# Kernel optimization log

Hardware: AMD Instinct MI355X
Metric: run time of the kernel (lower is better)

Reference implementation:

```python
import jax, jax.numpy as jnp
import numpy as np

DIM_NODE = 128
DIM_EDGE = 128
DIM_TIME = 100
NUM_HEAD = 8
DIM_OUT = 128
LN_EPS = 1e-5


def setup_inputs() -> dict:
    key = jax.random.key(0)
    ks = jax.random.split(key, 12)
    D, E = 25000, 250000
    src_feat = jax.random.normal(ks[0], (D + E, DIM_NODE), jnp.float32)
    edge_f = jax.random.normal(ks[1], (E, DIM_EDGE), jnp.float32)
    edge_dt = jax.random.uniform(ks[2], (E,), jnp.float32)
    src_idx = jnp.arange(D + E, dtype=jnp.int64)
    edge_dst = jnp.sort(jax.random.randint(ks[3], (E,), 0, D)).astype(jnp.int64)
    # TimeEncode params (fixed init from the module)
    time_w = jnp.asarray(1.0 / 10 ** np.linspace(0, 9, DIM_TIME, dtype=np.float32))  # (DIM_TIME,)
    time_b = jnp.zeros((DIM_TIME,), jnp.float32)
    dq = DIM_NODE + DIM_TIME           # 228
    dkv = DIM_NODE + DIM_EDGE + DIM_TIME  # 356
    s = 0.05
    wq_w = jax.random.normal(ks[4], (DIM_OUT, dq), jnp.float32) * s
    wq_b = jnp.zeros((DIM_OUT,), jnp.float32)
    wk_w = jax.random.normal(ks[5], (DIM_OUT, dkv), jnp.float32) * s
    wk_b = jnp.zeros((DIM_OUT,), jnp.float32)
    wv_w = jax.random.normal(ks[6], (DIM_OUT, dkv), jnp.float32) * s
    wv_b = jnp.zeros((DIM_OUT,), jnp.float32)
    wout_w = jax.random.normal(ks[7], (DIM_OUT, DIM_NODE + DIM_OUT), jnp.float32) * s
    wout_b = jnp.zeros((DIM_OUT,), jnp.float32)
    ln_g = jnp.ones((DIM_OUT,), jnp.float32)
    ln_b = jnp.zeros((DIM_OUT,), jnp.float32)
    return dict(src_feat=src_feat, edge_f=edge_f, edge_dt=edge_dt,
                time_w=time_w, time_b=time_b,
                wq_w=wq_w, wq_b=wq_b, wk_w=wk_w, wk_b=wk_b,
                wv_w=wv_w, wv_b=wv_b, wout_w=wout_w, wout_b=wout_b,
                ln_g=ln_g, ln_b=ln_b, src_idx=src_idx, edge_dst=edge_dst)


def reference(src_feat, edge_f, edge_dt, time_w, time_b,
              wq_w, wq_b, wk_w, wk_b, wv_w, wv_b,
              wout_w, wout_b, ln_g, ln_b, src_idx, edge_dst):
    E = edge_f.shape[0]
    src_data = src_feat[src_idx]              # (D+E, dn)
    D = src_data.shape[0] - E
    q_data = src_data[:D]                     # (D, dn)
    kv_data = src_data[D:]                    # (E, dn)

    # TimeEncode: cos(w * t + b)
    time_feat = jnp.cos(edge_dt[:, None] * time_w[None, :] + time_b)       # (E, dt)
    zero_time_feat = jnp.broadcast_to(jnp.cos(time_b), (D, DIM_TIME))      # (D, dt)

    Qd = jnp.concatenate([q_data, zero_time_feat], axis=1) @ wq_w.T + wq_b  # (D, dout)
    Q = Qd[edge_dst]                                                        # (E, dout)
    kv_in = jnp.concatenate([kv_data, edge_f, time_feat], axis=1)           # (E, dkv)
    K = kv_in @ wk_w.T + wk_b
    V = kv_in @ wv_w.T + wv_b

    dh = DIM_OUT // NUM_HEAD
    Q = Q.reshape(E, NUM_HEAD, dh)
    K = K.reshape(E, NUM_HEAD, dh)
    V = V.reshape(E, NUM_HEAD, dh)

    scores = jax.nn.leaky_relu(jnp.sum(Q * K, axis=2), 0.2)   # (E, H)
    # edge softmax: segment softmax over dst nodes
    m = jax.ops.segment_max(scores, edge_dst, num_segments=D)  # (D, H)
    m = jnp.where(jnp.isfinite(m), m, 0.0)
    ex = jnp.exp(scores - m[edge_dst])
    den = jax.ops.segment_sum(ex, edge_dst, num_segments=D)    # (D, H)
    att = ex / den[edge_dst]                                    # (E, H)

    Vw = (V * att[:, :, None]).reshape(E, DIM_OUT)
    h = jax.ops.segment_sum(Vw, edge_dst, num_segments=D)       # (D, dout)

    rst = jnp.concatenate([h, q_data], axis=1) @ wout_w.T + wout_b
    rst = jax.nn.relu(rst)
    mu = jnp.mean(rst, axis=-1, keepdims=True)
    var = jnp.var(rst, axis=-1, keepdims=True)
    return (rst - mu) / jnp.sqrt(var + LN_EPS) * ln_g + ln_b
```

## Files before the change

kernel.cpp:

```cpp
#include <hip/hip_runtime.h>
#include <stdint.h>

#define DIM_TIME 100
#define DQ 228
#define DKV 356
#define KPAD 384
#define NB 256
#define BM 64
#define BK 32
#define NCHUNK 12
#define A_STRIDE 392
#define C_STRIDE 264

typedef short v8s __attribute__((ext_vector_type(8)));
typedef float v4f __attribute__((ext_vector_type(4)));

__device__ __forceinline__ unsigned short bf16_bits(float f) {
    union { float f; uint32_t u; } c; c.f = f;
    uint32_t u = c.u;
    uint32_t r = (u + 0x7FFFu + ((u >> 16) & 1u)) >> 16;
    return (unsigned short)r;
}
__device__ __forceinline__ float bf16_lo(uint32_t u) {
    union { uint32_t u; float f; } c; c.u = u << 16; return c.f;
}
__device__ __forceinline__ float bf16_hi(uint32_t u) {
    union { uint32_t u; float f; } c; c.u = u & 0xFFFF0000u; return c.f;
}

__global__ void prep_wt2(const float* __restrict__ wk_w, const float* __restrict__ wv_w,
                         unsigned short* __restrict__ Wt2) {
    int n = blockIdx.x;
    int k = threadIdx.x;
    float v = 0.f;
    if (k < DKV) v = (n < 128) ? wk_w[n * DKV + k] : wv_w[(n - 128) * DKV + k];
    Wt2[n * KPAD + k] = bf16_bits(v);
}

__global__ void prep_wqt(const float* __restrict__ wq_w, float* __restrict__ Wqt) {
    int k = blockIdx.x, o = threadIdx.x;
    Wqt[k * 128 + o] = wq_w[o * DQ + k];
}

__global__ void prep_wot(const float* __restrict__ wout_w, float* __restrict__ Wot) {
    int k = blockIdx.x, o = threadIdx.x;
    Wot[k * 128 + o] = wout_w[o * 256 + k];
}

__global__ void prep_cq(const float* __restrict__ wq_w, const float* __restrict__ wq_b,
                        const float* __restrict__ time_b, float* __restrict__ cq) {
    int o = threadIdx.x;
    float s = wq_b[o];
    for (int t = 0; t < DIM_TIME; ++t)
        s += cosf(time_b[t]) * wq_w[o * DQ + 128 + t];
    cq[o] = s;
}

__global__ __launch_bounds__(256) void qd_kernel(
        const float* __restrict__ src_feat, const int* __restrict__ src_idx,
        const float* __restrict__ Wqt, const float* __restrict__ cq,
        float* __restrict__ Qd, int D) {
    __shared__ float q_s[32][128];
    int lane = threadIdx.x & 63, wave = threadIdx.x >> 6;
    int r0 = wave * 8;
    int d0 = blockIdx.x * 32 + r0;
    #pragma unroll
    for (int i = 0; i < 8; ++i) {
        int d = d0 + i;
        float v0 = 0.f, v1 = 0.f;
        if (d < D) {
            const float* p = src_feat + (size_t)src_idx[d] * 128;
            v0 = p[lane]; v1 = p[lane + 64];
        }
        q_s[r0 + i][lane] = v0; q_s[r0 + i][lane + 64] = v1;
    }
    float c0 = cq[lane], c1 = cq[lane + 64];
    float acc0[8], acc1[8];
    #pragma unroll
    for (int i = 0; i < 8; ++i) { acc0[i] = c0; acc1[i] = c1; }
    #pragma unroll 8
    for (int k = 0; k < 128; ++k) {
        float w0 = Wqt[k * 128 + lane];
        float w1 = Wqt[k * 128 + 64 + lane];
        #pragma unroll
        for (int i = 0; i < 8; ++i) {
            float a = q_s[r0 + i][k];
            acc0[i] += a * w0; acc1[i] += a * w1;
        }
    }
    #pragma unroll
    for (int i = 0; i < 8; ++i) {
        int d = d0 + i;
        if (d < D) {
            Qd[(size_t)d * 128 + lane]      = acc0[i];
            Qd[(size_t)d * 128 + 64 + lane] = acc1[i];
        }
    }
}

__global__ __launch_bounds__(256) void kv_mfma(
        const float* __restrict__ src_feat, const int* __restrict__ src_idx,
        const float* __restrict__ edge_f, const float* __restrict__ edge_dt,
        const float* __restrict__ time_w, const float* __restrict__ time_b,
        const unsigned short* __restrict__ Wt2,
        const float* __restrict__ wk_b, const float* __restrict__ wv_b,
        unsigned short* __restrict__ KVb, int D, int E) {
    __shared__ unsigned short A_s[BM * A_STRIDE];
    int tid = threadIdx.x;
    int e0 = blockIdx.x * BM;
    int lane = tid & 63, wave = tid >> 6;
    int l15 = lane & 15, quad = lane >> 4;
    int wn = wave * 64;

    {
        int row = tid >> 2;
        int cb  = (tid & 3) * 8;
        int e = e0 + row;
        bool ok = (e < E);
        size_t nbase = ok ? (size_t)src_idx[D + e] * 128 : 0;
        #pragma unroll
        for (int i = 0; i < 8; ++i) {
            int c4 = cb + i;
            float4 v = ok ? *(const float4*)(src_feat + nbase + c4 * 4)
                          : make_float4(0.f, 0.f, 0.f, 0.f);
            ushort4 w;
            w.x = bf16_bits(v.x); w.y = bf16_bits(v.y);
            w.z = bf16_bits(v.z); w.w = bf16_bits(v.w);
            *(ushort4*)&A_s[row * A_STRIDE + c4 * 4] = w;
        }
        #pragma unroll
        for (int i = 0; i < 8; ++i) {
            int c4 = cb + i;
            float4 v = ok ? *(const float4*)(edge_f + (size_t)e * 128 + c4 * 4)
                          : make_float4(0.f, 0.f, 0.f, 0.f);
            ushort4 w;
            w.x = bf16_bits(v.x); w.y = bf16_bits(v.y);
            w.z = bf16_bits(v.z); w.w = bf16_bits(v.w);
            *(ushort4*)&A_s[row * A_STRIDE + 128 + c4 * 4] = w;
        }
    }
    {
        int c = tid & 127;
        int rbase = tid >> 7;
        bool vc = (c < DIM_TIME);
        float tw = vc ? time_w[c] : 0.f;
        float tb = vc ? time_b[c] : 0.f;
        #pragma unroll
        for (int i = 0; i < 32; ++i) {
            int row = i * 2 + rbase;
            int e = e0 + row;
            float v = 0.f;
            if (vc && e < E) v = __cosf(edge_dt[e] * tw + tb);
            A_s[row * A_STRIDE + 256 + c] = bf16_bits(v);
        }
    }
    __syncthreads();

    v4f acc[4][4];
    #pragma unroll
    for (int mf = 0; mf < 4; ++mf)
        #pragma unroll
        for (int nf = 0; nf < 4; ++nf)
            acc[mf][nf] = (v4f)(0.f);

    const unsigned short* wp = Wt2 + (size_t)(wn + l15) * KPAD + quad * 8;
    const unsigned short* ap = A_s + l15 * A_STRIDE + quad * 8;

    v8s bcur[4], acur[4];
    #pragma unroll
    for (int nf = 0; nf < 4; ++nf) bcur[nf] = *(const v8s*)(wp + nf * 16 * KPAD);
    #pragma unroll
    for (int mf = 0; mf < 4; ++mf) acur[mf] = *(const v8s*)(ap + mf * 16 * A_STRIDE);

    #pragma unroll 2
    for (int ch = 0; ch < NCHUNK; ++ch) {
        int k2 = (ch + 1 < NCHUNK) ? (ch + 1) * BK : 0;
        v8s bn[4], an[4];
        #pragma unroll
        for (int nf = 0; nf < 4; ++nf) bn[nf] = *(const v8s*)(wp + nf * 16 * KPAD + k2);
        #pragma unroll
        for (int mf = 0; mf < 4; ++mf) an[mf] = *(const v8s*)(ap + mf * 16 * A_STRIDE + k2);
        #pragma unroll
        for (int mf = 0; mf < 4; ++mf)
            #pragma unroll
            for (int nf = 0; nf < 4; ++nf)
                acc[mf][nf] = __builtin_amdgcn_mfma_f32_16x16x32_bf16(
                                  acur[mf], bcur[nf], acc[mf][nf], 0, 0, 0);
        #pragma unroll
        for (int nf = 0; nf < 4; ++nf) bcur[nf] = bn[nf];
        #pragma unroll
        for (int mf = 0; mf < 4; ++mf) acur[mf] = an[mf];
    }

    __syncthreads();
    #pragma unroll
    for (int nf = 0; nf < 4; ++nf) {
        int n = wn + nf * 16 + l15;
        float bias = (n < 128) ? wk_b[n] : wv_b[n - 128];
        #pragma unroll
        for (int mf = 0; mf < 4; ++mf)
            #pragma unroll
            for (int r = 0; r < 4; ++r)
                A_s[(mf * 16 + quad * 4 + r) * C_STRIDE + n] =
                    bf16_bits(acc[mf][nf][r] + bias);
    }
    __syncthreads();
    #pragma unroll
    for (int j = 0; j < 8; ++j) {
        int c = j * 256 + tid;
        int row = c >> 5;
        int col = (c & 31) * 8;
        if (e0 + row < E) {
            v8s v = *(const v8s*)&A_s[row * C_STRIDE + col];
            *(v8s*)&KVb[(size_t)(e0 + row) * NB + col] = v;
        }
    }
}

__global__ void seg_offsets(const int* __restrict__ edge_dst, int* __restrict__ start,
                            int D, int E) {
    int d = blockIdx.x * blockDim.x + threadIdx.x;
    if (d > D) return;
    int lo = 0, hi = E;
    while (lo < hi) {
        int mid = (lo + hi) >> 1;
        if (edge_dst[mid] < d) lo = mid + 1; else hi = mid;
    }
    start[d] = lo;
}

__global__ __launch_bounds__(256) void attn_kernel(
        const float* __restrict__ Qd, const unsigned short* __restrict__ KVb,
        const int* __restrict__ start, float* __restrict__ h, int D) {
    int lane = threadIdx.x & 63, wave = threadIdx.x >> 6;
    int dbase = blockIdx.x * 16 + wave * 4;
    for (int i = 0; i < 4; ++i) {
        int d = dbase + i;
        if (d >= D) break;
        float2 q = *(const float2*)(Qd + (size_t)d * 128 + lane * 2);
        int s0 = start[d], s1 = start[d + 1];
        float m = -INFINITY, l = 0.f, a0 = 0.f, a1 = 0.f;
        for (int e = s0; e < s1; ++e) {
            const unsigned short* kv = KVb + (size_t)e * 256 + lane * 2;
            uint32_t ku = *(const uint32_t*)kv;
            uint32_t vu = *(const uint32_t*)(kv + 128);
            float qk = q.x * bf16_lo(ku) + q.y * bf16_hi(ku);
            qk += __shfl_xor(qk, 4, 8);
            qk += __shfl_xor(qk, 2, 8);
            qk += __shfl_xor(qk, 1, 8);
            float s = qk > 0.f ? qk : 0.2f * qk;
            float nm = fmaxf(m, s);
            float sc = __expf(m - nm);
            float p  = __expf(s - nm);
            l  = l  * sc + p;
            a0 = a0 * sc + p * bf16_lo(vu);
            a1 = a1 * sc + p * bf16_hi(vu);
            m = nm;
        }
        float inv = (l > 0.f) ? 1.f / l : 0.f;
        *(float2*)(h + (size_t)d * 128 + lane * 2) = make_float2(a0 * inv, a1 * inv);
    }
}

__global__ __launch_bounds__(256) void out_kernel(
        const float* __restrict__ h, const float* __restrict__ src_feat,
        const int* __restrict__ src_idx, const float* __restrict__ Wot,
        const float* __restrict__ wout_b, const float* __restrict__ ln_g,
        const float* __restrict__ ln_b, float* __restrict__ out, int D) {
    __shared__ float in_s[32][256];
    int lane = threadIdx.x & 63, wave = threadIdx.x >> 6;
    int r0 = wave * 8;
    int d0 = blockIdx.x * 32 + r0;
    #pragma unroll
    for (int i = 0; i < 8; ++i) {
        int d = d0 + i;
        float a0 = 0.f, a1 = 0.f, b0 = 0.f, b1 = 0.f;
        if (d < D) {
            const float* ph = h + (size_t)d * 128;
            a0 = ph[lane]; a1 = ph[lane + 64];
            const float* pf = src_feat + (size_t)src_idx[d] * 128;
            b0 = pf[lane]; b1 = pf[lane + 64];
        }
        in_s[r0 + i][lane] = a0; in_s[r0 + i][lane + 64] = a1;
        in_s[r0 + i][128 + lane] = b0; in_s[r0 + i][192 + lane] = b1;
    }
    float bb0 = wout_b[lane], bb1 = wout_b[lane + 64];
    float acc0[8], acc1[8];
    #pragma unroll
    for (int i = 0; i < 8; ++i) { acc0[i] = bb0; acc1[i] = bb1; }
    #pragma unroll 8
    for (int k = 0; k < 256; ++k) {
        float w0 = Wot[k * 128 + lane];
        float w1 = Wot[k * 128 + 64 + lane];
        #pragma unroll
        for (int i = 0; i < 8; ++i) {
            float a = in_s[r0 + i][k];
            acc0[i] += a * w0; acc1[i] += a * w1;
        }
    }
    float g0 = ln_g[lane], g1 = ln_g[lane + 64];
    float lb0 = ln_b[lane], lb1 = ln_b[lane + 64];
    #pragma unroll
    for (int i = 0; i < 8; ++i) {
        float v0 = fmaxf(acc0[i], 0.f), v1 = fmaxf(acc1[i], 0.f);
        float s1 = v0 + v1, s2 = v0 * v0 + v1 * v1;
        #pragma unroll
        for (int off = 32; off; off >>= 1) {
            s1 += __shfl_xor(s1, off);
            s2 += __shfl_xor(s2, off);
        }
        float mu  = s1 * (1.f / 128.f);
        float var = s2 * (1.f / 128.f) - mu * mu;
        float rs  = rsqrtf(var + 1e-5f);
        int d = d0 + i;
        if (d < D) {
            out[(size_t)d * 128 + lane]      = (v0 - mu) * rs * g0 + lb0;
            out[(size_t)d * 128 + 64 + lane] = (v1 - mu) * rs * g1 + lb1;
        }
    }
}

extern "C" void kernel_launch(void* const* d_in, const int* in_sizes, int n_in,
                              void* d_out, int out_size, void* d_ws, size_t ws_size,
                              hipStream_t stream) {
    const float* src_feat = (const float*)d_in[0];
    const float* edge_f   = (const float*)d_in[1];
    const float* edge_dt  = (const float*)d_in[2];
    const float* time_w   = (const float*)d_in[3];
    const float* time_b   = (const float*)d_in[4];
    const float* wq_w     = (const float*)d_in[5];
    const float* wq_b     = (const float*)d_in[6];
    const float* wk_w     = (const float*)d_in[7];
    const float* wk_b     = (const float*)d_in[8];
    const float* wv_w     = (const float*)d_in[9];
    const float* wv_b     = (const float*)d_in[10];
    const float* wout_w   = (const float*)d_in[11];
    const float* wout_b   = (const float*)d_in[12];
    const float* ln_g     = (const float*)d_in[13];
    const float* ln_b     = (const float*)d_in[14];
    const int*   src_idx  = (const int*)d_in[15];
    const int*   edge_dst = (const int*)d_in[16];

    int DE = in_sizes[0] / 128;
    int E  = in_sizes[1] / 128;
    int D  = DE - E;

    char* ws = (char*)d_ws;
    size_t off = 0;
    auto alloc = [&](size_t bytes) {
        void* p = ws + off;
        off = (off + bytes + 511) & ~(size_t)511;
        return p;
    };
    unsigned short* Wt2   = (unsigned short*)alloc((size_t)NB * KPAD * 2);
    float*          Wqt   = (float*)alloc(128 * 128 * 4);
    float*          Wot   = (float*)alloc(256 * 128 * 4);
    float*          cq    = (float*)alloc(128 * 4);
    float*          Qd    = (float*)alloc((size_t)D * 128 * 4);
    unsigned short* KVb   = (unsigned short*)alloc((size_t)E * 256 * 2);
    float*          hb    = (float*)alloc((size_t)D * 128 * 4);
    int*            start = (int*)alloc((size_t)(D + 1) * 4);

    hipLaunchKernelGGL(prep_wt2, dim3(NB), dim3(KPAD), 0, stream, wk_w, wv_w, Wt2);
    hipLaunchKernelGGL(prep_wqt, dim3(128), dim3(128), 0, stream, wq_w, Wqt);
    hipLaunchKernelGGL(prep_wot, dim3(256), dim3(128), 0, stream, wout_w, Wot);
    hipLaunchKernelGGL(prep_cq, dim3(1), dim3(128), 0, stream, wq_w, wq_b, time_b, cq);
    hipLaunchKernelGGL(qd_kernel, dim3((D + 31) / 32), dim3(256), 0, stream,
                       src_feat, src_idx, Wqt, cq, Qd, D);
    hipLaunchKernelGGL(kv_mfma, dim3((E + BM - 1) / BM), dim3(256), 0, stream,
                       src_feat, src_idx, edge_f, edge_dt, time_w, time_b,
                       Wt2, wk_b, wv_b, KVb, D, E);
    hipLaunchKernelGGL(seg_offsets, dim3((D + 1 + 255) / 256), dim3(256), 0, stream,
                       edge_dst, start, D, E);
    hipLaunchKernelGGL(attn_kernel, dim3((D + 15) / 16), dim3(256), 0, stream,
                       Qd, KVb, start, hb, D);
    hipLaunchKernelGGL(out_kernel, dim3((D + 31) / 32), dim3(256), 0, stream,
                       hb, src_feat, src_idx, Wot, wout_b, ln_g, ln_b, (float*)d_out, D);
}
```

Baseline: 640.0 us.

## Halve KV GEMM tile rows, batch attention KV loads, vectorize small GEMM loads

The KV projection kernel now uses 32-row tiles instead of 64, which doubles the block count and gives more blocks per CU for latency hiding, at the cost of reusing each weight fragment less. The attention kernel issues up to four edges' K/V loads before the serial online-softmax updates, so memory latency overlaps across edges. The Q and output projection kernels switch to float2 loads and stores for weights, biases and outputs, with each lane now owning adjacent column pairs. The launch config for the KV kernel presumably already derives its grid from BM.

```diff
diff --git a/kernel.cpp b/kernel.cpp
--- a/kernel.cpp
+++ b/kernel.cpp
@@ -6,7 +6,7 @@
 #define DKV 356
 #define KPAD 384
 #define NB 256
-#define BM 64
+#define BM 32
 #define BK 32
 #define NCHUNK 12
 #define A_STRIDE 392
@@ -74,27 +74,24 @@
         }
         q_s[r0 + i][lane] = v0; q_s[r0 + i][lane + 64] = v1;
     }
-    float c0 = cq[lane], c1 = cq[lane + 64];
+    float2 c2 = *(const float2*)(cq + 2 * lane);
     float acc0[8], acc1[8];
     #pragma unroll
-    for (int i = 0; i < 8; ++i) { acc0[i] = c0; acc1[i] = c1; }
+    for (int i = 0; i < 8; ++i) { acc0[i] = c2.x; acc1[i] = c2.y; }
     #pragma unroll 8
     for (int k = 0; k < 128; ++k) {
-        float w0 = Wqt[k * 128 + lane];
-        float w1 = Wqt[k * 128 + 64 + lane];
+        float2 w = *(const float2*)(Wqt + k * 128 + 2 * lane);
         #pragma unroll
         for (int i = 0; i < 8; ++i) {
             float a = q_s[r0 + i][k];
-            acc0[i] += a * w0; acc1[i] += a * w1;
+            acc0[i] += a * w.x; acc1[i] += a * w.y;
         }
     }
     #pragma unroll
     for (int i = 0; i < 8; ++i) {
         int d = d0 + i;
-        if (d < D) {
-            Qd[(size_t)d * 128 + lane]      = acc0[i];
-            Qd[(size_t)d * 128 + 64 + lane] = acc1[i];
-        }
+        if (d < D)
+            *(float2*)(Qd + (size_t)d * 128 + 2 * lane) = make_float2(acc0[i], acc1[i]);
     }
 }
 
@@ -113,13 +110,13 @@
     int wn = wave * 64;
 
     {
-        int row = tid >> 2;
-        int cb  = (tid & 3) * 8;
+        int row = tid >> 3;
+        int cb  = (tid & 7) * 4;
         int e = e0 + row;
         bool ok = (e < E);
         size_t nbase = ok ? (size_t)src_idx[D + e] * 128 : 0;
         #pragma unroll
-        for (int i = 0; i < 8; ++i) {
+        for (int i = 0; i < 4; ++i) {
             int c4 = cb + i;
             float4 v = ok ? *(const float4*)(src_feat + nbase + c4 * 4)
                           : make_float4(0.f, 0.f, 0.f, 0.f);
@@ -129,7 +126,7 @@
             *(ushort4*)&A_s[row * A_STRIDE + c4 * 4] = w;
         }
         #pragma unroll
-        for (int i = 0; i < 8; ++i) {
+        for (int i = 0; i < 4; ++i) {
             int c4 = cb + i;
             float4 v = ok ? *(const float4*)(edge_f + (size_t)e * 128 + c4 * 4)
                           : make_float4(0.f, 0.f, 0.f, 0.f);
@@ -146,7 +143,7 @@
         float tw = vc ? time_w[c] : 0.f;
         float tb = vc ? time_b[c] : 0.f;
         #pragma unroll
-        for (int i = 0; i < 32; ++i) {
+        for (int i = 0; i < 16; ++i) {
             int row = i * 2 + rbase;
             int e = e0 + row;
             float v = 0.f;
@@ -156,9 +153,9 @@
     }
     __syncthreads();
 
-    v4f acc[4][4];
-    #pragma unroll
-    for (int mf = 0; mf < 4; ++mf)
+    v4f acc[2][4];
+    #pragma unroll
+    for (int mf = 0; mf < 2; ++mf)
         #pragma unroll
         for (int nf = 0; nf < 4; ++nf)
             acc[mf][nf] = (v4f)(0.f);
@@ -166,22 +163,22 @@
     const unsigned short* wp = Wt2 + (size_t)(wn + l15) * KPAD + quad * 8;
     const unsigned short* ap = A_s + l15 * A_STRIDE + quad * 8;
 
-    v8s bcur[4], acur[4];
+    v8s bcur[4], acur[2];
     #pragma unroll
     for (int nf = 0; nf < 4; ++nf) bcur[nf] = *(const v8s*)(wp + nf * 16 * KPAD);
     #pragma unroll
-    for (int mf = 0; mf < 4; ++mf) acur[mf] = *(const v8s*)(ap + mf * 16 * A_STRIDE);
+    for (int mf = 0; mf < 2; ++mf) acur[mf] = *(const v8s*)(ap + mf * 16 * A_STRIDE);
 
     #pragma unroll 2
     for (int ch = 0; ch < NCHUNK; ++ch) {
         int k2 = (ch + 1 < NCHUNK) ? (ch + 1) * BK : 0;
-        v8s bn[4], an[4];
+        v8s bn[4], an[2];
         #pragma unroll
         for (int nf = 0; nf < 4; ++nf) bn[nf] = *(const v8s*)(wp + nf * 16 * KPAD + k2);
         #pragma unroll
-        for (int mf = 0; mf < 4; ++mf) an[mf] = *(const v8s*)(ap + mf * 16 * A_STRIDE + k2);
-        #pragma unroll
-        for (int mf = 0; mf < 4; ++mf)
+        for (int mf = 0; mf < 2; ++mf) an[mf] = *(const v8s*)(ap + mf * 16 * A_STRIDE + k2);
+        #pragma unroll
+        for (int mf = 0; mf < 2; ++mf)
             #pragma unroll
             for (int nf = 0; nf < 4; ++nf)
                 acc[mf][nf] = __builtin_amdgcn_mfma_f32_16x16x32_bf16(
@@ -189,7 +186,7 @@
         #pragma unroll
         for (int nf = 0; nf < 4; ++nf) bcur[nf] = bn[nf];
         #pragma unroll
-        for (int mf = 0; mf < 4; ++mf) acur[mf] = an[mf];
+        for (int mf = 0; mf < 2; ++mf) acur[mf] = an[mf];
     }
 
     __syncthreads();
@@ -198,7 +195,7 @@
         int n = wn + nf * 16 + l15;
         float bias = (n < 128) ? wk_b[n] : wv_b[n - 128];
         #pragma unroll
-        for (int mf = 0; mf < 4; ++mf)
+        for (int mf = 0; mf < 2; ++mf)
             #pragma unroll
             for (int r = 0; r < 4; ++r)
                 A_s[(mf * 16 + quad * 4 + r) * C_STRIDE + n] =
@@ -206,7 +203,7 @@
     }
     __syncthreads();
     #pragma unroll
-    for (int j = 0; j < 8; ++j) {
+    for (int j = 0; j < 4; ++j) {
         int c = j * 256 + tid;
         int row = c >> 5;
         int col = (c & 31) * 8;
@@ -240,22 +237,31 @@
         float2 q = *(const float2*)(Qd + (size_t)d * 128 + lane * 2);
         int s0 = start[d], s1 = start[d + 1];
         float m = -INFINITY, l = 0.f, a0 = 0.f, a1 = 0.f;
-        for (int e = s0; e < s1; ++e) {
-            const unsigned short* kv = KVb + (size_t)e * 256 + lane * 2;
-            uint32_t ku = *(const uint32_t*)kv;
-            uint32_t vu = *(const uint32_t*)(kv + 128);
-            float qk = q.x * bf16_lo(ku) + q.y * bf16_hi(ku);
-            qk += __shfl_xor(qk, 4, 8);
-            qk += __shfl_xor(qk, 2, 8);
-            qk += __shfl_xor(qk, 1, 8);
-            float s = qk > 0.f ? qk : 0.2f * qk;
-            float nm = fmaxf(m, s);
-            float sc = __expf(m - nm);
-            float p  = __expf(s - nm);
-            l  = l  * sc + p;
-            a0 = a0 * sc + p * bf16_lo(vu);
-            a1 = a1 * sc + p * bf16_hi(vu);
-            m = nm;
+        for (int e = s0; e < s1; e += 4) {
+            int n = s1 - e; if (n > 4) n = 4;
+            uint32_t ku[4], vu[4];
+            #pragma unroll
+            for (int j = 0; j < 4; ++j) {
+                if (j < n) {
+                    const unsigned short* kv = KVb + (size_t)(e + j) * 256 + lane * 2;
+                    ku[j] = *(const uint32_t*)kv;
+                    vu[j] = *(const uint32_t*)(kv + 128);
+                }
+            }
+            for (int j = 0; j < n; ++j) {
+                float qk = q.x * bf16_lo(ku[j]) + q.y * bf16_hi(ku[j]);
+                qk += __shfl_xor(qk, 4, 8);
+                qk += __shfl_xor(qk, 2, 8);
+                qk += __shfl_xor(qk, 1, 8);
+                float s = qk > 0.f ? qk : 0.2f * qk;
+                float nm = fmaxf(m, s);
+                float sc = __expf(m - nm);
+                float p  = __expf(s - nm);
+                l  = l  * sc + p;
+                a0 = a0 * sc + p * bf16_lo(vu[j]);
+                a1 = a1 * sc + p * bf16_hi(vu[j]);
+                m = nm;
+            }
         }
         float inv = (l > 0.f) ? 1.f / l : 0.f;
         *(float2*)(h + (size_t)d * 128 + lane * 2) = make_float2(a0 * inv, a1 * inv);
@@ -284,22 +290,21 @@
         in_s[r0 + i][lane] = a0; in_s[r0 + i][lane + 64] = a1;
         in_s[r0 + i][128 + lane] = b0; in_s[r0 + i][192 + lane] = b1;
     }
-    float bb0 = wout_b[lane], bb1 = wout_b[lane + 64];
+    float2 bb = *(const float2*)(wout_b + 2 * lane);
     float acc0[8], acc1[8];
     #pragma unroll
-    for (int i = 0; i < 8; ++i) { acc0[i] = bb0; acc1[i] = bb1; }
+    for (int i = 0; i < 8; ++i) { acc0[i] = bb.x; acc1[i] = bb.y; }
     #pragma unroll 8
     for (int k = 0; k < 256; ++k) {
-        float w0 = Wot[k * 128 + lane];
-        float w1 = Wot[k * 128 + 64 + lane];
+        float2 w = *(const float2*)(Wot + k * 128 + 2 * lane);
         #pragma unroll
         for (int i = 0; i < 8; ++i) {
             float a = in_s[r0 + i][k];
-            acc0[i] += a * w0; acc1[i] += a * w1;
-        }
-    }
-    float g0 = ln_g[lane], g1 = ln_g[lane + 64];
-    float lb0 = ln_b[lane], lb1 = ln_b[lane + 64];
+            acc0[i] += a * w.x; acc1[i] += a * w.y;
+        }
+    }
+    float2 g = *(const float2*)(ln_g + 2 * lane);
+    float2 lb = *(const float2*)(ln_b + 2 * lane);
     #pragma unroll
     for (int i = 0; i < 8; ++i) {
         float v0 = fmaxf(acc0[i], 0.f), v1 = fmaxf(acc1[i], 0.f);
@@ -313,10 +318,9 @@
         float var = s2 * (1.f / 128.f) - mu * mu;
         float rs  = rsqrtf(var + 1e-5f);
         int d = d0 + i;
-        if (d < D) {
-            out[(size_t)d * 128 + lane]      = (v0 - mu) * rs * g0 + lb0;
-            out[(size_t)d * 128 + 64 + lane] = (v1 - mu) * rs * g1 + lb1;
-        }
+        if (d < D)
+            *(float2*)(out + (size_t)d * 128 + 2 * lane) =
+                make_float2((v0 - mu) * rs * g.x + lb.x, (v1 - mu) * rs * g.y + lb.y);
     }
 }
 
```

Measured after the change: 672.8 us. 5.1% more time.
